# Kernel tuning notes

Hardware: AMD Instinct MI355X
Metric: run time of the kernel (lower is better)

## Reference

```python
import jax, jax.numpy as jnp
import numpy as np

WINDOWS = (5, 10, 20)
EPS = 1e-4
K_SLICES = 3
OVERLAP = 0.5


def setup_inputs() -> dict:
    key = jax.random.key(0)
    k1, k2, k3, k4 = jax.random.split(key, 4)
    B, T, H = 64, 2048, 256
    x = jax.random.normal(k1, (B, T, H), dtype=jnp.float32)
    alpha = 0.1 * jax.random.normal(k2, (H, len(WINDOWS)), dtype=jnp.float32)
    gamma = 1.0 + 0.1 * jax.random.normal(k3, (K_SLICES, H), dtype=jnp.float32)
    beta = 0.1 * jax.random.normal(k4, (K_SLICES, H), dtype=jnp.float32)
    return {"x": x, "alpha": alpha, "gamma": gamma, "beta": beta}


def _fan(x, alpha):
    # FrequencyAdaptiveNormSimple: multi-window sliding mean/std, blended by softmax(alpha).
    B, T, H = x.shape
    al = jax.nn.softmax(alpha, axis=-1)  # [H, nW]
    # prefix sums for O(T) sliding statistics (same math as unfold mean/std)
    zrow = jnp.zeros((B, 1, H), x.dtype)
    S1 = jnp.concatenate([zrow, jnp.cumsum(x, axis=1)], axis=1)        # [B, T+1, H]
    S2 = jnp.concatenate([zrow, jnp.cumsum(x * x, axis=1)], axis=1)    # [B, T+1, H]
    out = jnp.zeros_like(x)
    for wi, w in enumerate(WINDOWS):
        if w > T:
            continue
        ws = S1[:, w:, :] - S1[:, : T - w + 1, :]    # window sums, [B, T-w+1, H]
        ws2 = S2[:, w:, :] - S2[:, : T - w + 1, :]
        mu = ws / w
        var = jnp.maximum((ws2 - ws * ws / w) / (w - 1), 0.0)  # unbiased (torch std default)
        sd = jnp.maximum(jnp.sqrt(var), EPS)
        # F.pad(..., (w-1, 0), mode='replicate') on the time dim
        mu = jnp.pad(mu, ((0, 0), (w - 1, 0), (0, 0)), mode="edge")
        sd = jnp.pad(sd, ((0, 0), (w - 1, 0), (0, 0)), mode="edge")
        z = jnp.nan_to_num((x - mu) / sd, nan=0.0, posinf=0.0, neginf=0.0)
        out = out + z * al[:, wi][None, None, :]
    return out


def _san(x, gamma, beta):
    # SliceAdaptiveNormSimple: overlapping slices, per-slice (B,T) stats (detached), affine, avg.
    B, T, H = x.shape
    step = max(1, int(round(T / (K_SLICES - (K_SLICES - 1) * OVERLAP))))
    win = min(T, step + int(round(step * OVERLAP)))
    y = jnp.zeros_like(x)
    cnt = jnp.zeros((B, T, 1), x.dtype)
    s = 0
    for k in range(K_SLICES):
        e = min(T, s + win)
        if e <= s:
            break
        xk = x[:, s:e, :]
        mu = jax.lax.stop_gradient(jnp.mean(xk, axis=(0, 1), keepdims=True))
        sd = jax.lax.stop_gradient(
            jnp.maximum(jnp.std(xk, axis=(0, 1), ddof=1, keepdims=True), 1e-4)
        )
        z = jnp.nan_to_num((xk - mu) / sd, nan=0.0, posinf=0.0, neginf=0.0)
        z = z * gamma[k][None, None, :] + beta[k][None, None, :]
        y = y.at[:, s:e, :].add(z)
        cnt = cnt.at[:, s:e, :].add(1.0)
        s += step
    return y / (cnt + EPS)


def reference(x, alpha, gamma, beta):
    # StableFANSAN: out = x + SAN(FAN(x))
    return x + _san(_fan(x, alpha), gamma, beta)
```

## Files before the change

kernel.cpp:

```cpp
#include <hip/hip_runtime.h>
#include <hip/hip_fp16.h>

#define T_DIM 2048
#define H_DIM 256
#define B_DIM 64

#define FCH 64
#define FNCH (T_DIM / FCH)
#define FNCB (B_DIM * FNCH)

#define ECH 64
#define ENCH (T_DIM / ECH)
#define ENCB (B_DIM * ENCH)

#define EPS_F 1e-4f
#define R1C (1.0f / 1.0001f)
#define R2C (1.0f / 2.0001f)

__device__ __forceinline__ void win_stats(float s1, float s2, float inv_w, float inv_wm1,
                                          float& mu, float& isd) {
    mu = s1 * inv_w;
    float var = fmaxf((s2 - s1 * s1 * inv_w) * inv_wm1, 0.0f);
    isd = fminf(rsqrtf(var), 1e4f);
}

template <int MODE, bool FIRST>
__device__ __forceinline__ void run_chunk(
    const float* __restrict__ xbh, __half2* __restrict__ s2bh, float* __restrict__ s32bh,
    int t0, float al0, float al1, float al2,
    float& ls1, float& ls2,
    float mu5i, float isd5i, float mu10i, float isd10i, float mu20i, float isd20i) {

    float s1_5 = 0.f, s2_5 = 0.f, s1_10 = 0.f, s2_10 = 0.f, s1_20 = 0.f, s2_20 = 0.f;
    float hist[16];
    float fprev = 0.0f;

    if (FIRST) {
#pragma unroll
        for (int j = 0; j < 16; ++j) hist[j] = 0.0f;
    } else {
#pragma unroll
        for (int j = 1; j <= 20; ++j) {
            float v = xbh[(t0 - j) * H_DIM];
            s1_20 += v; s2_20 += v * v;
            if (j <= 10) { s1_10 += v; s2_10 += v * v; hist[(16 - j) & 15] = v; }
            if (j <= 5)  { s1_5  += v; s2_5  += v * v; }
        }
    }

    for (int i0 = 0; i0 < FCH; i0 += 32) {
#pragma unroll
        for (int k = 0; k < 32; ++k) {
            const int t = t0 + i0 + k;
            const float v = xbh[t * H_DIM];
            float o20 = 0.0f;
            if (!FIRST || i0 + k >= 20) o20 = xbh[(t - 20) * H_DIM];
            s1_5  += v; s2_5  += v * v;
            s1_10 += v; s2_10 += v * v;
            s1_20 += v; s2_20 += v * v;
            if (!FIRST || i0 + k >= 5)  { float o = hist[(k - 5)  & 15]; s1_5  -= o; s2_5  -= o * o; }
            if (!FIRST || i0 + k >= 10) { float o = hist[(k - 10) & 15]; s1_10 -= o; s2_10 -= o * o; }
            if (!FIRST || i0 + k >= 20) { s1_20 -= o20; s2_20 -= o20 * o20; }
            hist[k & 15] = v;

            float mu, isd, fan = 0.0f;
            if (!FIRST || i0 + k >= 4)  win_stats(s1_5,  s2_5,  0.2f,  0.25f,      mu, isd);
            else { mu = mu5i;  isd = isd5i; }
            fan += (v - mu) * isd * al0;
            if (!FIRST || i0 + k >= 9)  win_stats(s1_10, s2_10, 0.1f,  1.f / 9.f,  mu, isd);
            else { mu = mu10i; isd = isd10i; }
            fan += (v - mu) * isd * al1;
            if (!FIRST || i0 + k >= 19) win_stats(s1_20, s2_20, 0.05f, 1.f / 19.f, mu, isd);
            else { mu = mu20i; isd = isd20i; }
            fan += (v - mu) * isd * al2;

            ls1 += fan; ls2 += fan * fan;
            if (MODE == 0) {
                if (k & 1) s2bh[(size_t)(t >> 1) * H_DIM] =
                               __halves2half2(__float2half(fprev), __float2half(fan));
                else       fprev = fan;
            } else {
                s32bh[t * H_DIM] = fan;
            }
        }
    }
}

template <int MODE>
__global__ __launch_bounds__(256)
void fan_kernel(const float* __restrict__ x, const float* __restrict__ alpha,
                float* __restrict__ part, __half* __restrict__ stash16,
                float* __restrict__ stash32) {
    const int blk = (blockIdx.x & 7) * (FNCB / 8) + (blockIdx.x >> 3);
    const int b = blk / FNCH;
    const int c = blk % FNCH;
    const int h = threadIdx.x;
    const int t0 = c * FCH;
    const size_t base = (size_t)b * T_DIM * H_DIM + h;
    const float* xbh = x + base;
    __half2* s2bh = (MODE == 0)
        ? (__half2*)stash16 + (size_t)b * (T_DIM / 2) * H_DIM + h : nullptr;
    float* s32bh = (MODE == 1) ? stash32 + base : nullptr;

    const float a0 = alpha[h * 3 + 0], a1 = alpha[h * 3 + 1], a2 = alpha[h * 3 + 2];
    const float mx = fmaxf(a0, fmaxf(a1, a2));
    const float e0 = __expf(a0 - mx), e1 = __expf(a1 - mx), e2 = __expf(a2 - mx);
    const float einv = 1.0f / (e0 + e1 + e2);
    const float al0 = e0 * einv, al1 = e1 * einv, al2 = e2 * einv;

    float ls1 = 0.0f, ls2 = 0.0f;

    if (c == 0) {
        float mu5i, isd5i, mu10i, isd10i, mu20i, isd20i;
        float c1 = 0.f, c2 = 0.f;
#pragma unroll
        for (int j = 0; j < 20; ++j) {
            float v = xbh[j * H_DIM];
            c1 += v; c2 += v * v;
            if (j == 4)  win_stats(c1, c2, 0.2f,  0.25f,      mu5i,  isd5i);
            if (j == 9)  win_stats(c1, c2, 0.1f,  1.f / 9.f,  mu10i, isd10i);
            if (j == 19) win_stats(c1, c2, 0.05f, 1.f / 19.f, mu20i, isd20i);
        }
        run_chunk<MODE, true>(xbh, s2bh, s32bh, t0, al0, al1, al2, ls1, ls2,
                              mu5i, isd5i, mu10i, isd10i, mu20i, isd20i);
    } else {
        run_chunk<MODE, false>(xbh, s2bh, s32bh, t0, al0, al1, al2, ls1, ls2,
                               0.f, 0.f, 0.f, 0.f, 0.f, 0.f);
    }

    part[(0 * FNCB + blk) * H_DIM + h] = ls1;
    part[(1 * FNCB + blk) * H_DIM + h] = ls2;
}

__global__ __launch_bounds__(256)
void reduce_kernel(const float* __restrict__ part, float* __restrict__ part2) {
    const int h = threadIdx.x;
    const int k = blockIdx.x >> 4;
    const int g = blockIdx.x & 15;
    float a1 = 0.f, a2 = 0.f;
    for (int i = 0; i < FNCB / 16; ++i) {
        const int blk = g * (FNCB / 16) + i;
        const int c = blk % FNCH;
        const bool member = (k == 0) ? (c < 24) : (c >= 16);
        if (member) {
            a1 += part[(0 * FNCB + blk) * H_DIM + h];
            a2 += part[(1 * FNCB + blk) * H_DIM + h];
        }
    }
    part2[((2 * k + 0) * 16 + g) * H_DIM + h] = a1;
    part2[((2 * k + 1) * 16 + g) * H_DIM + h] = a2;
}

template <bool HALF>
__global__ __launch_bounds__(256)
void epilogue_kernel(const float* __restrict__ x, const void* __restrict__ fanp,
                     const float* __restrict__ part2, const float* __restrict__ gamma,
                     const float* __restrict__ beta, float* __restrict__ out) {
    __shared__ __align__(16) float cf[4][H_DIM];
    const int tid = threadIdx.x;

    {
        float S10 = 0.f, S20 = 0.f, S11 = 0.f, S21 = 0.f;
#pragma unroll
        for (int g = 0; g < 16; ++g) {
            S10 += part2[(0 * 16 + g) * H_DIM + tid];
            S20 += part2[(1 * 16 + g) * H_DIM + tid];
            S11 += part2[(2 * 16 + g) * H_DIM + tid];
            S21 += part2[(3 * 16 + g) * H_DIM + tid];
        }
        const float N0 = 64.0f * 1536.0f, N1 = 64.0f * 1024.0f;
        float mu0 = S10 / N0;
        float v0 = fmaxf((S20 - S10 * S10 / N0) / (N0 - 1.0f), 0.0f);
        float isd0 = 1.0f / fmaxf(sqrtf(v0), EPS_F);
        float mu1 = S11 / N1;
        float v1 = fmaxf((S21 - S11 * S11 / N1) / (N1 - 1.0f), 0.0f);
        float isd1 = 1.0f / fmaxf(sqrtf(v1), EPS_F);
        float A0 = isd0 * gamma[0 * H_DIM + tid];
        float A1 = isd1 * gamma[1 * H_DIM + tid];
        cf[0][tid] = A0;
        cf[1][tid] = beta[0 * H_DIM + tid] - mu0 * A0;
        cf[2][tid] = A1;
        cf[3][tid] = beta[1 * H_DIM + tid] - mu1 * A1;
    }
    __syncthreads();

    const int blk = blockIdx.x;
    const int b = blk / ENCH;
    const int c = blk % ENCH;
    const int wave = tid >> 6;
    const int lane = tid & 63;
    const int h4 = lane * 4;

    float4 A0 = *(const float4*)&cf[0][h4];
    float4 B0 = *(const float4*)&cf[1][h4];
    float4 A1 = *(const float4*)&cf[2][h4];
    float4 B1 = *(const float4*)&cf[3][h4];
    float4 A, Bv;
    if (c < 16) {
        A  = make_float4(A0.x * R1C, A0.y * R1C, A0.z * R1C, A0.w * R1C);
        Bv = make_float4(B0.x * R1C, B0.y * R1C, B0.z * R1C, B0.w * R1C);
    } else if (c >= 24) {
        A  = make_float4(A1.x * R1C, A1.y * R1C, A1.z * R1C, A1.w * R1C);
        Bv = make_float4(B1.x * R1C, B1.y * R1C, B1.z * R1C, B1.w * R1C);
    } else {
        A  = make_float4((A0.x + A1.x) * R2C, (A0.y + A1.y) * R2C, (A0.z + A1.z) * R2C, (A0.w + A1.w) * R2C);
        Bv = make_float4((B0.x + B1.x) * R2C, (B0.y + B1.y) * R2C, (B0.z + B1.z) * R2C, (B0.w + B1.w) * R2C);
    }

    const int tbase = c * ECH + wave * 16;
    if (HALF) {
        const __half2* s2 = (const __half2*)fanp + (size_t)b * (T_DIM / 2) * H_DIM + h4;
#pragma unroll 2
        for (int p = 0; p < 8; ++p) {
            const int t = tbase + 2 * p;
            const size_t xi = ((size_t)b * T_DIM + t) * H_DIM + h4;
            float4 x0 = *(const float4*)&x[xi];
            float4 x1 = *(const float4*)&x[xi + H_DIM];
            float4 sv = *(const float4*)(s2 + (size_t)(t >> 1) * H_DIM);
            __half2 q0 = *reinterpret_cast<const __half2*>(&sv.x);
            __half2 q1 = *reinterpret_cast<const __half2*>(&sv.y);
            __half2 q2 = *reinterpret_cast<const __half2*>(&sv.z);
            __half2 q3 = *reinterpret_cast<const __half2*>(&sv.w);
            float4 o0, o1;
            o0.x = x0.x + fmaf(__low2float(q0),  A.x, Bv.x);
            o0.y = x0.y + fmaf(__low2float(q1),  A.y, Bv.y);
            o0.z = x0.z + fmaf(__low2float(q2),  A.z, Bv.z);
            o0.w = x0.w + fmaf(__low2float(q3),  A.w, Bv.w);
            o1.x = x1.x + fmaf(__high2float(q0), A.x, Bv.x);
            o1.y = x1.y + fmaf(__high2float(q1), A.y, Bv.y);
            o1.z = x1.z + fmaf(__high2float(q2), A.z, Bv.z);
            o1.w = x1.w + fmaf(__high2float(q3), A.w, Bv.w);
            *(float4*)&out[xi] = o0;
            *(float4*)&out[xi + H_DIM] = o1;
        }
    } else {
#pragma unroll 4
        for (int i = 0; i < 16; ++i) {
            const size_t idx = ((size_t)b * T_DIM + tbase + i) * H_DIM + h4;
            float4 xv = *(const float4*)&x[idx];
            float4 fv = *(const float4*)&((const float*)fanp)[idx];
            float4 o;
            o.x = xv.x + fmaf(fv.x, A.x, Bv.x);
            o.y = xv.y + fmaf(fv.y, A.y, Bv.y);
            o.z = xv.z + fmaf(fv.z, A.z, Bv.z);
            o.w = xv.w + fmaf(fv.w, A.w, Bv.w);
            *(float4*)&out[idx] = o;
        }
    }
}

extern "C" void kernel_launch(void* const* d_in, const int* in_sizes, int n_in,
                              void* d_out, int out_size, void* d_ws, size_t ws_size,
                              hipStream_t stream) {
    const float* x     = (const float*)d_in[0];
    const float* alpha = (const float*)d_in[1];
    const float* gamma = (const float*)d_in[2];
    const float* beta  = (const float*)d_in[3];
    float* out  = (float*)d_out;

    float* part  = (float*)d_ws;
    float* part2 = part + 2 * FNCB * H_DIM;
    __half* stash16 = (__half*)(part2 + 64 * H_DIM);
    const size_t need = (size_t)(2 * FNCB * H_DIM + 64 * H_DIM) * 4
                      + (size_t)B_DIM * T_DIM * H_DIM * 2;
    const bool half_path = (ws_size >= need);

    if (half_path) {
        fan_kernel<0><<<FNCB, H_DIM, 0, stream>>>(x, alpha, part, stash16, nullptr);
    } else {
        fan_kernel<1><<<FNCB, H_DIM, 0, stream>>>(x, alpha, part, nullptr, out);
    }
    reduce_kernel<<<32, H_DIM, 0, stream>>>(part, part2);
    if (half_path) {
        epilogue_kernel<true><<<ENCB, 256, 0, stream>>>(x, stash16, part2, gamma, beta, out);
    } else {
        epilogue_kernel<false><<<ENCB, 256, 0, stream>>>(x, out, part2, gamma, beta, out);
    }
}
```

Before: 352.3 us.

## Stage FAN input rows in an LDS ring buffer via async global-to-LDS loads

The FAN kernel no longer reads each x element and its window-expiry values (t-5, t-10, t-20) straight from global memory per thread. It streams rows of x into a 32-row shared-memory ring buffer with global_load_lds, one wave per row, and reads both the new and the expiring values from LDS. This removes the redundant global/L2 reads of the lagged samples and the register history array. In exchange it adds two block barriers every 8 rows, and the prefetch distance is short, so much of the load latency may still be exposed.

```diff
diff --git a/kernel.cpp b/kernel.cpp
--- a/kernel.cpp
+++ b/kernel.cpp
@@ -16,6 +16,9 @@
 #define EPS_F 1e-4f
 #define R1C (1.0f / 1.0001f)
 #define R2C (1.0f / 2.0001f)
+
+#define GLB(p) ((const __attribute__((address_space(1))) void*)(p))
+#define LDSP(p) ((__attribute__((address_space(3))) void*)(p))
 
 __device__ __forceinline__ void win_stats(float s1, float s2, float inv_w, float inv_wm1,
                                           float& mu, float& isd) {
@@ -25,64 +28,73 @@
 }
 
 template <int MODE, bool FIRST>
-__device__ __forceinline__ void run_chunk(
-    const float* __restrict__ xbh, __half2* __restrict__ s2bh, float* __restrict__ s32bh,
-    int t0, float al0, float al1, float al2,
-    float& ls1, float& ls2,
+__device__ __forceinline__ void run_main(
+    float (*xs)[H_DIM], const float* __restrict__ xb, int t0, int h, int wave, int lane,
+    __half2* __restrict__ s2bh, float* __restrict__ s32bh,
+    float al0, float al1, float al2, float& ls1, float& ls2,
     float mu5i, float isd5i, float mu10i, float isd10i, float mu20i, float isd20i) {
 
     float s1_5 = 0.f, s2_5 = 0.f, s1_10 = 0.f, s2_10 = 0.f, s1_20 = 0.f, s2_20 = 0.f;
-    float hist[16];
+
+    if (!FIRST) {
+#pragma unroll
+        for (int j = 1; j <= 20; ++j) {
+            float v = xs[(-j) & 31][h];
+            s1_20 += v; s2_20 += v * v;
+            if (j <= 10) { s1_10 += v; s2_10 += v * v; }
+            if (j <= 5)  { s1_5  += v; s2_5  += v * v; }
+        }
+    }
+
     float fprev = 0.0f;
-
-    if (FIRST) {
-#pragma unroll
-        for (int j = 0; j < 16; ++j) hist[j] = 0.0f;
-    } else {
-#pragma unroll
-        for (int j = 1; j <= 20; ++j) {
-            float v = xbh[(t0 - j) * H_DIM];
-            s1_20 += v; s2_20 += v * v;
-            if (j <= 10) { s1_10 += v; s2_10 += v * v; hist[(16 - j) & 15] = v; }
-            if (j <= 5)  { s1_5  += v; s2_5  += v * v; }
-        }
-    }
-
-    for (int i0 = 0; i0 < FCH; i0 += 32) {
-#pragma unroll
-        for (int k = 0; k < 32; ++k) {
-            const int t = t0 + i0 + k;
-            const float v = xbh[t * H_DIM];
-            float o20 = 0.0f;
-            if (!FIRST || i0 + k >= 20) o20 = xbh[(t - 20) * H_DIM];
+    for (int g = 0; g < 8; ++g) {
+#pragma unroll
+        for (int j = 0; j < 8; ++j) {
+            const int rl = 8 * g + j;
+            const int t = t0 + rl;
+            const float v = xs[rl & 31][h];
+
             s1_5  += v; s2_5  += v * v;
             s1_10 += v; s2_10 += v * v;
             s1_20 += v; s2_20 += v * v;
-            if (!FIRST || i0 + k >= 5)  { float o = hist[(k - 5)  & 15]; s1_5  -= o; s2_5  -= o * o; }
-            if (!FIRST || i0 + k >= 10) { float o = hist[(k - 10) & 15]; s1_10 -= o; s2_10 -= o * o; }
-            if (!FIRST || i0 + k >= 20) { s1_20 -= o20; s2_20 -= o20 * o20; }
-            hist[k & 15] = v;
+            if (!FIRST || rl >= 5)  { float o = xs[(rl - 5)  & 31][h]; s1_5  -= o; s2_5  -= o * o; }
+            if (!FIRST || rl >= 10) { float o = xs[(rl - 10) & 31][h]; s1_10 -= o; s2_10 -= o * o; }
+            if (!FIRST || rl >= 20) { float o = xs[(rl - 20) & 31][h]; s1_20 -= o; s2_20 -= o * o; }
 
             float mu, isd, fan = 0.0f;
-            if (!FIRST || i0 + k >= 4)  win_stats(s1_5,  s2_5,  0.2f,  0.25f,      mu, isd);
+            if (!FIRST || rl >= 4)  win_stats(s1_5,  s2_5,  0.2f,  0.25f,      mu, isd);
             else { mu = mu5i;  isd = isd5i; }
             fan += (v - mu) * isd * al0;
-            if (!FIRST || i0 + k >= 9)  win_stats(s1_10, s2_10, 0.1f,  1.f / 9.f,  mu, isd);
+            if (!FIRST || rl >= 9)  win_stats(s1_10, s2_10, 0.1f,  1.f / 9.f,  mu, isd);
             else { mu = mu10i; isd = isd10i; }
             fan += (v - mu) * isd * al1;
-            if (!FIRST || i0 + k >= 19) win_stats(s1_20, s2_20, 0.05f, 1.f / 19.f, mu, isd);
+            if (!FIRST || rl >= 19) win_stats(s1_20, s2_20, 0.05f, 1.f / 19.f, mu, isd);
             else { mu = mu20i; isd = isd20i; }
             fan += (v - mu) * isd * al2;
 
             ls1 += fan; ls2 += fan * fan;
             if (MODE == 0) {
-                if (k & 1) s2bh[(size_t)(t >> 1) * H_DIM] =
+                if (j & 1) s2bh[(size_t)(t >> 1) * H_DIM] =
                                __halves2half2(__float2half(fprev), __float2half(fan));
                 else       fprev = fan;
             } else {
                 s32bh[t * H_DIM] = fan;
             }
         }
+        if (g < 7) {
+            __syncthreads();
+            const int rl0 = 8 * g + 12 + 2 * wave;
+#pragma unroll
+            for (int j = 0; j < 2; ++j) {
+                const int rl = rl0 + j;
+                if (rl < FCH) {
+                    __builtin_amdgcn_global_load_lds(
+                        GLB(xb + (size_t)(t0 + rl) * H_DIM + lane * 4),
+                        LDSP(&xs[rl & 31][0]), 16, 0, 0);
+                }
+            }
+            __syncthreads();
+        }
     }
 }
 
@@ -91,16 +103,32 @@
 void fan_kernel(const float* __restrict__ x, const float* __restrict__ alpha,
                 float* __restrict__ part, __half* __restrict__ stash16,
                 float* __restrict__ stash32) {
+    __shared__ __align__(16) float xs[32][H_DIM];
     const int blk = (blockIdx.x & 7) * (FNCB / 8) + (blockIdx.x >> 3);
     const int b = blk / FNCH;
     const int c = blk % FNCH;
     const int h = threadIdx.x;
+    const int wave = h >> 6;
+    const int lane = h & 63;
     const int t0 = c * FCH;
-    const size_t base = (size_t)b * T_DIM * H_DIM + h;
-    const float* xbh = x + base;
+    const size_t base = (size_t)b * T_DIM * H_DIM;
+    const float* xb = x + base;
     __half2* s2bh = (MODE == 0)
         ? (__half2*)stash16 + (size_t)b * (T_DIM / 2) * H_DIM + h : nullptr;
-    float* s32bh = (MODE == 1) ? stash32 + base : nullptr;
+    float* s32bh = (MODE == 1) ? stash32 + base + h : nullptr;
+
+    {
+        const int rl0 = -20 + 8 * wave;
+#pragma unroll
+        for (int j = 0; j < 8; ++j) {
+            const int rl = rl0 + j;
+            if (t0 + rl >= 0) {
+                __builtin_amdgcn_global_load_lds(
+                    GLB(xb + (size_t)(t0 + rl) * H_DIM + lane * 4),
+                    LDSP(&xs[rl & 31][0]), 16, 0, 0);
+            }
+        }
+    }
 
     const float a0 = alpha[h * 3 + 0], a1 = alpha[h * 3 + 1], a2 = alpha[h * 3 + 2];
     const float mx = fmaxf(a0, fmaxf(a1, a2));
@@ -115,17 +143,21 @@
         float c1 = 0.f, c2 = 0.f;
 #pragma unroll
         for (int j = 0; j < 20; ++j) {
-            float v = xbh[j * H_DIM];
+            float v = xb[j * H_DIM + h];
             c1 += v; c2 += v * v;
             if (j == 4)  win_stats(c1, c2, 0.2f,  0.25f,      mu5i,  isd5i);
             if (j == 9)  win_stats(c1, c2, 0.1f,  1.f / 9.f,  mu10i, isd10i);
             if (j == 19) win_stats(c1, c2, 0.05f, 1.f / 19.f, mu20i, isd20i);
         }
-        run_chunk<MODE, true>(xbh, s2bh, s32bh, t0, al0, al1, al2, ls1, ls2,
-                              mu5i, isd5i, mu10i, isd10i, mu20i, isd20i);
-    } else {
-        run_chunk<MODE, false>(xbh, s2bh, s32bh, t0, al0, al1, al2, ls1, ls2,
-                               0.f, 0.f, 0.f, 0.f, 0.f, 0.f);
+        __syncthreads();
+        run_main<MODE, true>(xs, xb, t0, h, wave, lane, s2bh, s32bh,
+                             al0, al1, al2, ls1, ls2,
+                             mu5i, isd5i, mu10i, isd10i, mu20i, isd20i);
+    } else {
+        __syncthreads();
+        run_main<MODE, false>(xs, xb, t0, h, wave, lane, s2bh, s32bh,
+                              al0, al1, al2, ls1, ls2,
+                              0.f, 0.f, 0.f, 0.f, 0.f, 0.f);
     }
 
     part[(0 * FNCB + blk) * H_DIM + h] = ls1;
```

After: 343.5 us. 1.03x faster.
